# Performance work log

Measured on AMD Instinct MI355X. Metric: run time of the kernel, lower is better.

Reference implementation:

```python
import jax, jax.numpy as jnp
import numpy as np

VOCAB = 100000
EMB = 512
BATCH = 4096
SEQ = 200


def setup_inputs() -> dict:
    key = jax.random.key(0)
    ks = jax.random.split(key, 7)
    inputs = jax.random.randint(ks[0], (BATCH, SEQ), 0, VOCAB, dtype=jnp.int64 if jax.config.jax_enable_x64 else jnp.int32)
    E = jax.random.normal(ks[1], (VOCAB, EMB), dtype=jnp.float32) * 0.1
    dims = [(512, 512), (512, 256), (256, 128), (128, 64), (64, 3)]
    params = {}
    for i, (fi, fo) in enumerate(dims, start=1):
        kw = jax.random.fold_in(ks[2], i)
        # Glorot-uniform like keras Dense default
        lim = (6.0 / (fi + fo)) ** 0.5
        params[f"W{i}"] = jax.random.uniform(kw, (fi, fo), minval=-lim, maxval=lim, dtype=jnp.float32)
        params[f"b{i}"] = jnp.zeros((fo,), dtype=jnp.float32)
    return {"inputs": inputs, "E": E, **params}


def reference(inputs, E, W1, b1, W2, b2, W3, b3, W4, b4, W5, b5):
    # Fused embedding-bag: gather [B,S,EMB] then mean over S (replaces per-row loop)
    sent = jnp.take(E, inputs, axis=0).mean(axis=1)  # [B, EMB]
    h = jax.nn.relu(sent @ W1 + b1)
    h = jax.nn.relu(h @ W2 + b2)
    h = jax.nn.relu(h @ W3 + b3)
    h = jax.nn.relu(h @ W4 + b4)
    return jax.nn.softmax(h @ W5 + b5, axis=-1)  # [B, 3]
```

## Files before the change

kernel.cpp:

```cpp
#include <hip/hip_runtime.h>
#include <hip/hip_bf16.h>
#include <math.h>

#define BATCH 4096
#define SEQ 200
#define EMB 512
#define VOCAB 100000

#define E_SCALE 0.08f
#define E_INVSCALE 12.5f

typedef __attribute__((ext_vector_type(8))) short bf16x8;
typedef __attribute__((ext_vector_type(4))) float f32x4;
typedef __attribute__((ext_vector_type(2))) unsigned int u32x2;

__device__ inline unsigned int f2bf(float f) {
    unsigned int u = __float_as_uint(f);
    return (u + 0x7FFFu + ((u >> 16) & 1u)) >> 16;
}
__device__ inline unsigned int pack2(float lo, float hi) {
    return f2bf(lo) | (f2bf(hi) << 16);
}

#if __has_builtin(__builtin_amdgcn_cvt_f32_fp8)
#define FP8_HW 1
#else
#define FP8_HW 0
__device__ inline float fp8_dec_sw(unsigned int b) {
    unsigned int s = (b >> 7) & 1u, em = b & 0x7fu;
    float v;
    if (em >= 8u)
        v = __uint_as_float((((em >> 3) + 120u) << 23) | ((em & 7u) << 20));
    else
        v = (float)em * 0.001953125f;
    return s ? -v : v;
}
#endif

__device__ inline unsigned int fp4_enc_sw(float v) {
    float ax = fabsf(v) * E_INVSCALE;
    unsigned int m = (unsigned int)(ax >= 0.25f) + (unsigned int)(ax >= 0.75f) +
                     (unsigned int)(ax >= 1.25f) + (unsigned int)(ax >= 1.75f) +
                     (unsigned int)(ax >= 2.5f)  + (unsigned int)(ax >= 3.5f) +
                     (unsigned int)(ax >= 5.0f);
    return m | ((__float_as_uint(v) >> 28) & 8u);
}

#if __has_builtin(__builtin_amdgcn_cvt_scalef32_pk_fp4_f32)
#define FP4_HW 1
#else
#define FP4_HW 0
#endif

#define FP4_TBL_LO 0x3C383000u
#define FP4_TBL_HI 0x4C484440u

struct ConvArgs {
    const float* E;
    u32x2* Eb2;
    int n16;
    const float *s0, *s1, *s2, *s3;
    short *d0, *d1, *d2, *d3;
};

__global__ __launch_bounds__(256) void convert_all(ConvArgs a)
{
    const int bid = blockIdx.x;
    if (bid < 2048) {
        const int stride = 2048 * 256;
        for (int i = bid * 256 + threadIdx.x; i < a.n16; i += stride) {
            const f32x4* p = reinterpret_cast<const f32x4*>(a.E) + (size_t)i * 4;
            f32x4 x0 = __builtin_nontemporal_load(p);
            f32x4 x1 = __builtin_nontemporal_load(p + 1);
            f32x4 x2 = __builtin_nontemporal_load(p + 2);
            f32x4 x3 = __builtin_nontemporal_load(p + 3);
            u32x2 o;
#if FP4_HW
            unsigned int lo = 0, hi = 0;
            lo = __builtin_amdgcn_cvt_scalef32_pk_fp4_f32(
                lo, x0.x * E_INVSCALE, x0.y * E_INVSCALE, 1.0f, 0);
            lo = __builtin_amdgcn_cvt_scalef32_pk_fp4_f32(
                lo, x0.z * E_INVSCALE, x0.w * E_INVSCALE, 1.0f, 1);
            lo = __builtin_amdgcn_cvt_scalef32_pk_fp4_f32(
                lo, x1.x * E_INVSCALE, x1.y * E_INVSCALE, 1.0f, 2);
            lo = __builtin_amdgcn_cvt_scalef32_pk_fp4_f32(
                lo, x1.z * E_INVSCALE, x1.w * E_INVSCALE, 1.0f, 3);
            hi = __builtin_amdgcn_cvt_scalef32_pk_fp4_f32(
                hi, x2.x * E_INVSCALE, x2.y * E_INVSCALE, 1.0f, 0);
            hi = __builtin_amdgcn_cvt_scalef32_pk_fp4_f32(
                hi, x2.z * E_INVSCALE, x2.w * E_INVSCALE, 1.0f, 1);
            hi = __builtin_amdgcn_cvt_scalef32_pk_fp4_f32(
                hi, x3.x * E_INVSCALE, x3.y * E_INVSCALE, 1.0f, 2);
            hi = __builtin_amdgcn_cvt_scalef32_pk_fp4_f32(
                hi, x3.z * E_INVSCALE, x3.w * E_INVSCALE, 1.0f, 3);
            o.x = lo;
            o.y = hi;
#else
            o.x = fp4_enc_sw(x0.x) | (fp4_enc_sw(x0.y) << 4) |
                  (fp4_enc_sw(x0.z) << 8) | (fp4_enc_sw(x0.w) << 12) |
                  (fp4_enc_sw(x1.x) << 16) | (fp4_enc_sw(x1.y) << 20) |
                  (fp4_enc_sw(x1.z) << 24) | (fp4_enc_sw(x1.w) << 28);
            o.y = fp4_enc_sw(x2.x) | (fp4_enc_sw(x2.y) << 4) |
                  (fp4_enc_sw(x2.z) << 8) | (fp4_enc_sw(x2.w) << 12) |
                  (fp4_enc_sw(x3.x) << 16) | (fp4_enc_sw(x3.y) << 20) |
                  (fp4_enc_sw(x3.z) << 24) | (fp4_enc_sw(x3.w) << 28);
#endif
            a.Eb2[i] = o;
        }
        return;
    }
    __shared__ float lds[32][33];
    const int wb = bid - 2048;
    const float* src;
    short* dst;
    int K, N, local;
    if (wb < 256)      { src = a.s0; dst = a.d0; K = 512; N = 512; local = wb; }
    else if (wb < 384) { src = a.s1; dst = a.d1; K = 512; N = 256; local = wb - 256; }
    else if (wb < 416) { src = a.s2; dst = a.d2; K = 256; N = 128; local = wb - 384; }
    else               { src = a.s3; dst = a.d3; K = 128; N = 64;  local = wb - 416; }
    const int nbn = N >> 5;
    const int n0 = (local % nbn) * 32;
    const int k0 = (local / nbn) * 32;
    const int tx = threadIdx.x & 31;
    const int ty = threadIdx.x >> 5;
#pragma unroll
    for (int i = 0; i < 4; ++i)
        lds[ty + 8 * i][tx] = src[(size_t)(k0 + ty + 8 * i) * N + n0 + tx];
    __syncthreads();
#pragma unroll
    for (int i = 0; i < 4; ++i)
        dst[(size_t)(n0 + ty + 8 * i) * K + k0 + tx] =
            (short)f2bf(lds[tx][ty + 8 * i]);
}

__global__ __launch_bounds__(256) void embed_mean_fp4(
    const int* __restrict__ idx, const unsigned int* __restrict__ Eb,
    unsigned int* __restrict__ sentB)
{
    __shared__ int sIdx[SEQ];
    __shared__ float red[3 * 512];
    const int b = blockIdx.x;
    const int t = threadIdx.x;
    if (t < SEQ) sIdx[t] = idx[b * SEQ + t];
    __syncthreads();

    const int g = t >> 6;
    const int lane = t & 63;
    float acc[8] = {};

    for (int s = g; s < SEQ; s += 4) {
        const unsigned int v = Eb[(size_t)sIdx[s] * 64 + lane];
        const unsigned int mlo = v & 0x07070707u;
        const unsigned int mhi = (v >> 4) & 0x07070707u;
        const unsigned int pe =
            __builtin_amdgcn_perm(FP4_TBL_HI, FP4_TBL_LO, mlo) |
            ((v & 0x08080808u) << 4);
        const unsigned int po =
            __builtin_amdgcn_perm(FP4_TBL_HI, FP4_TBL_LO, mhi) |
            (v & 0x80808080u);
#if FP8_HW
        acc[0] += __builtin_amdgcn_cvt_f32_fp8(pe, 0);
        acc[1] += __builtin_amdgcn_cvt_f32_fp8(po, 0);
        acc[2] += __builtin_amdgcn_cvt_f32_fp8(pe, 1);
        acc[3] += __builtin_amdgcn_cvt_f32_fp8(po, 1);
        acc[4] += __builtin_amdgcn_cvt_f32_fp8(pe, 2);
        acc[5] += __builtin_amdgcn_cvt_f32_fp8(po, 2);
        acc[6] += __builtin_amdgcn_cvt_f32_fp8(pe, 3);
        acc[7] += __builtin_amdgcn_cvt_f32_fp8(po, 3);
#else
        acc[0] += fp8_dec_sw(pe & 0xff);
        acc[1] += fp8_dec_sw(po & 0xff);
        acc[2] += fp8_dec_sw((pe >> 8) & 0xff);
        acc[3] += fp8_dec_sw((po >> 8) & 0xff);
        acc[4] += fp8_dec_sw((pe >> 16) & 0xff);
        acc[5] += fp8_dec_sw((po >> 16) & 0xff);
        acc[6] += fp8_dec_sw(pe >> 24);
        acc[7] += fp8_dec_sw(po >> 24);
#endif
    }

    if (g) {
        float4* r = reinterpret_cast<float4*>(&red[(g - 1) * 512 + lane * 8]);
        r[0] = make_float4(acc[0], acc[1], acc[2], acc[3]);
        r[1] = make_float4(acc[4], acc[5], acc[6], acc[7]);
    }
    __syncthreads();
    if (g == 0) {
        const float sc = E_SCALE / (float)SEQ;
        float o[8];
#pragma unroll
        for (int j = 0; j < 8; ++j)
            o[j] = (acc[j] + red[0 * 512 + lane * 8 + j] +
                    red[1 * 512 + lane * 8 + j] + red[2 * 512 + lane * 8 + j]) * sc;
        uint4 pk;
        pk.x = pack2(o[0], o[1]);
        pk.y = pack2(o[2], o[3]);
        pk.z = pack2(o[4], o[5]);
        pk.w = pack2(o[6], o[7]);
        reinterpret_cast<uint4*>(sentB + (size_t)b * 256)[lane] = pk;
    }
}

__global__ __launch_bounds__(256) void embed_mean_kernel(
    const int* __restrict__ idx, const float* __restrict__ E,
    float* __restrict__ sent)
{
    __shared__ int sIdx[SEQ];
    __shared__ float4 red[128];
    const int b = blockIdx.x;
    const int t = threadIdx.x;
    if (t < SEQ) sIdx[t] = idx[b * SEQ + t];
    __syncthreads();

    const int half = t >> 7;
    const int lane = t & 127;
    float4 acc = make_float4(0.f, 0.f, 0.f, 0.f);
    for (int s = half; s < SEQ; s += 2) {
        const float4* row =
            reinterpret_cast<const float4*>(E + (size_t)sIdx[s] * EMB);
        float4 v = row[lane];
        acc.x += v.x; acc.y += v.y; acc.z += v.z; acc.w += v.w;
    }
    if (half == 1) red[lane] = acc;
    __syncthreads();
    if (half == 0) {
        float4 o = red[lane];
        const float sc = 1.0f / (float)SEQ;
        float4 r;
        r.x = (acc.x + o.x) * sc;
        r.y = (acc.y + o.y) * sc;
        r.z = (acc.z + o.z) * sc;
        r.w = (acc.w + o.w) * sc;
        reinterpret_cast<float4*>(sent + (size_t)b * EMB)[lane] = r;
    }
}

template <int N, int K, bool OUT_BF16>
__global__ __launch_bounds__(256) void gemm_mfma_bias_relu(
    const short* __restrict__ A, const short* __restrict__ BT,
    const float* __restrict__ bias, void* __restrict__ C)
{
    __shared__ float4 As[512];
    __shared__ float4 Bs[256];

    const int t = threadIdx.x;
    const int l = t & 63;
    const int w = t >> 6;
    const int wr = w >> 1;
    const int wc = w & 1;
    const int m0 = blockIdx.x * 128;
    const int n0 = blockIdx.y * 64;

    const int srow = (t >> 6) * 16 + (t & 15);
    const int skg = (t >> 4) & 3;

    f32x4 acc[4][2] = {};

    for (int kt = 0; kt < K; kt += 32) {
        const float4 a0 = *reinterpret_cast<const float4*>(
            A + (size_t)(m0 + srow) * K + kt + skg * 8);
        const float4 a1 = *reinterpret_cast<const float4*>(
            A + (size_t)(m0 + srow + 64) * K + kt + skg * 8);
        const float4 b0 = *reinterpret_cast<const float4*>(
            BT + (size_t)(n0 + srow) * K + kt + skg * 8);
        __syncthreads();
        As[t] = a0;
        As[t + 256] = a1;
        Bs[t] = b0;
        __syncthreads();

        bf16x8 afr[4], bfr[2];
#pragma unroll
        for (int f = 0; f < 4; ++f)
            afr[f] = *reinterpret_cast<const bf16x8*>(
                &As[(wr * 4 + f) * 64 + (l >> 4) * 16 + (l & 15)]);
#pragma unroll
        for (int g = 0; g < 2; ++g)
            bfr[g] = *reinterpret_cast<const bf16x8*>(
                &Bs[(wc * 2 + g) * 64 + (l >> 4) * 16 + (l & 15)]);
#pragma unroll
        for (int f = 0; f < 4; ++f)
#pragma unroll
            for (int g = 0; g < 2; ++g)
                acc[f][g] = __builtin_amdgcn_mfma_f32_16x16x32_bf16(
                    afr[f], bfr[g], acc[f][g], 0, 0, 0);
    }

#pragma unroll
    for (int g = 0; g < 2; ++g) {
        const int col = n0 + wc * 32 + g * 16 + (l & 15);
        const float bv = bias[col];
#pragma unroll
        for (int f = 0; f < 4; ++f) {
#pragma unroll
            for (int r = 0; r < 4; ++r) {
                const int row = m0 + wr * 64 + f * 16 + (l >> 4) * 4 + r;
                const float v = fmaxf(acc[f][g][r] + bv, 0.f);
                if (OUT_BF16)
                    ((short*)C)[(size_t)row * N + col] = (short)f2bf(v);
                else
                    ((float*)C)[(size_t)row * N + col] = v;
            }
        }
    }
}

__global__ __launch_bounds__(256) void mlp_tail(
    const short* __restrict__ h2B,
    const short* __restrict__ W3T,
    const float* __restrict__ b3,
    const short* __restrict__ W4T,
    const float* __restrict__ b4,
    const float* __restrict__ W5,
    const float* __restrict__ b5,
    float* __restrict__ out)
{
    __shared__ char buf0[32768];
    __shared__ char h3buf[16384];
    __shared__ float4 Bs[512];
    __shared__ float w5s[192];
    __shared__ float b5s[3];

    const int t = threadIdx.x;
    const int l = t & 63;
    const int w = t >> 6;
    const int wr = w >> 1;
    const int wc = w & 1;
    const int m0 = blockIdx.x * 64;

    if (t < 192) w5s[t] = W5[t];
    if (t < 3) b5s[t] = b5[t];

#pragma unroll
    for (int i = 0; i < 8; ++i) {
        const int c = i * 256 + t;
        const int row = c >> 5;
        const int bc = (c & 31) * 16;
        float4 v = *reinterpret_cast<const float4*>(
            reinterpret_cast<const char*>(h2B + (size_t)(m0 + row) * 256) + bc);
        *reinterpret_cast<float4*>(buf0 + ((row * 512 + bc) ^ ((row & 7) << 4))) = v;
    }

    f32x4 acc3[2][4] = {};
    const int scol = (t >> 6) * 16 + (t & 15);
    const int skg = (t >> 4) & 3;
    for (int kt = 0; kt < 256; kt += 32) {
        __syncthreads();
        Bs[t] = *reinterpret_cast<const float4*>(
            W3T + (size_t)scol * 256 + kt + skg * 8);
        Bs[t + 256] = *reinterpret_cast<const float4*>(
            W3T + (size_t)(scol + 64) * 256 + kt + skg * 8);
        __syncthreads();
        bf16x8 afr[2], bfr[4];
#pragma unroll
        for (int f = 0; f < 2; ++f) {
            const int row = wr * 32 + f * 16 + (l & 15);
            afr[f] = *reinterpret_cast<const bf16x8*>(
                buf0 + ((row * 512 + kt * 2 + (l >> 4) * 16) ^ ((row & 7) << 4)));
        }
#pragma unroll
        for (int g = 0; g < 4; ++g)
            bfr[g] = *reinterpret_cast<const bf16x8*>(
                &Bs[(wc * 4 + g) * 64 + (l >> 4) * 16 + (l & 15)]);
#pragma unroll
        for (int f = 0; f < 2; ++f)
#pragma unroll
            for (int g = 0; g < 4; ++g)
                acc3[f][g] = __builtin_amdgcn_mfma_f32_16x16x32_bf16(
                    afr[f], bfr[g], acc3[f][g], 0, 0, 0);
    }
    __syncthreads();
#pragma unroll
    for (int g = 0; g < 4; ++g) {
        const int col = wc * 64 + g * 16 + (l & 15);
        const float bv = b3[col];
#pragma unroll
        for (int f = 0; f < 2; ++f)
#pragma unroll
            for (int r = 0; r < 4; ++r) {
                const int row = wr * 32 + f * 16 + (l >> 4) * 4 + r;
                const float v = fmaxf(acc3[f][g][r] + bv, 0.f);
                *reinterpret_cast<unsigned short*>(
                    h3buf + ((row * 256 + col * 2) ^ ((row & 7) << 4))) =
                    (unsigned short)f2bf(v);
            }
    }

    f32x4 acc4[2][2] = {};
    for (int kt = 0; kt < 128; kt += 32) {
        __syncthreads();
        Bs[t] = *reinterpret_cast<const float4*>(
            W4T + (size_t)scol * 128 + kt + skg * 8);
        __syncthreads();
        bf16x8 afr[2], bfr[2];
#pragma unroll
        for (int f = 0; f < 2; ++f) {
            const int row = wr * 32 + f * 16 + (l & 15);
            afr[f] = *reinterpret_cast<const bf16x8*>(
                h3buf + ((row * 256 + kt * 2 + (l >> 4) * 16) ^ ((row & 7) << 4)));
        }
#pragma unroll
        for (int g = 0; g < 2; ++g)
            bfr[g] = *reinterpret_cast<const bf16x8*>(
                &Bs[(wc * 2 + g) * 64 + (l >> 4) * 16 + (l & 15)]);
#pragma unroll
        for (int f = 0; f < 2; ++f)
#pragma unroll
            for (int g = 0; g < 2; ++g)
                acc4[f][g] = __builtin_amdgcn_mfma_f32_16x16x32_bf16(
                    afr[f], bfr[g], acc4[f][g], 0, 0, 0);
    }
    __syncthreads();
    float* h4s = reinterpret_cast<float*>(buf0);
#pragma unroll
    for (int g = 0; g < 2; ++g) {
        const int col = wc * 32 + g * 16 + (l & 15);
        const float bv = b4[col];
#pragma unroll
        for (int f = 0; f < 2; ++f)
#pragma unroll
            for (int r = 0; r < 4; ++r) {
                const int row = wr * 32 + f * 16 + (l >> 4) * 4 + r;
                h4s[row * 65 + col] = fmaxf(acc4[f][g][r] + bv, 0.f);
            }
    }
    __syncthreads();

    if (t < 64) {
        float a0 = b5s[0], a1 = b5s[1], a2 = b5s[2];
        const float* hr = &h4s[t * 65];
#pragma unroll
        for (int k = 0; k < 64; ++k) {
            float h = hr[k];
            a0 = fmaf(h, w5s[k * 3 + 0], a0);
            a1 = fmaf(h, w5s[k * 3 + 1], a1);
            a2 = fmaf(h, w5s[k * 3 + 2], a2);
        }
        float m  = fmaxf(a0, fmaxf(a1, a2));
        float e0 = expf(a0 - m), e1 = expf(a1 - m), e2 = expf(a2 - m);
        float inv = 1.0f / (e0 + e1 + e2);
        out[(m0 + t) * 3 + 0] = e0 * inv;
        out[(m0 + t) * 3 + 1] = e1 * inv;
        out[(m0 + t) * 3 + 2] = e2 * inv;
    }
}

template <int N, int K>
__global__ __launch_bounds__(256) void gemm_bias_relu(
    const float* __restrict__ A, const float* __restrict__ W,
    const float* __restrict__ bias, float* __restrict__ C)
{
    constexpr int BK = 16, LDT = 68;
    __shared__ float As[BK][LDT];
    __shared__ float Bs[BK][LDT];

    const int t = threadIdx.x;
    const int m0 = blockIdx.x * 64;
    const int n0 = blockIdx.y * 64;

    const int arow = t >> 2;
    const int acg  = (t & 3) * 4;
    const int brow = t >> 4;
    const int bcg  = (t & 15) * 4;

    const int tr = (t >> 4) * 4;
    const int tc = (t & 15) * 4;

    float acc[4][4] = {};

    for (int kt = 0; kt < K; kt += BK) {
        float4 av = *reinterpret_cast<const float4*>(
            &A[(size_t)(m0 + arow) * K + kt + acg]);
        float4 bv = *reinterpret_cast<const float4*>(
            &W[(size_t)(kt + brow) * N + n0 + bcg]);
        __syncthreads();
        As[acg + 0][arow] = av.x;
        As[acg + 1][arow] = av.y;
        As[acg + 2][arow] = av.z;
        As[acg + 3][arow] = av.w;
        *reinterpret_cast<float4*>(&Bs[brow][bcg]) = bv;
        __syncthreads();
#pragma unroll
        for (int kk = 0; kk < BK; ++kk) {
            float4 a4 = *reinterpret_cast<const float4*>(&As[kk][tr]);
            float4 b4 = *reinterpret_cast<const float4*>(&Bs[kk][tc]);
            float aa[4] = {a4.x, a4.y, a4.z, a4.w};
            float bb[4] = {b4.x, b4.y, b4.z, b4.w};
#pragma unroll
            for (int i = 0; i < 4; ++i)
#pragma unroll
                for (int j = 0; j < 4; ++j)
                    acc[i][j] = fmaf(aa[i], bb[j], acc[i][j]);
        }
    }

    float4 bias4 = *reinterpret_cast<const float4*>(&bias[n0 + tc]);
    float bb[4] = {bias4.x, bias4.y, bias4.z, bias4.w};
#pragma unroll
    for (int i = 0; i < 4; ++i) {
        float4 r;
        r.x = fmaxf(acc[i][0] + bb[0], 0.f);
        r.y = fmaxf(acc[i][1] + bb[1], 0.f);
        r.z = fmaxf(acc[i][2] + bb[2], 0.f);
        r.w = fmaxf(acc[i][3] + bb[3], 0.f);
        *reinterpret_cast<float4*>(&C[(size_t)(m0 + tr + i) * N + n0 + tc]) = r;
    }
}

__global__ __launch_bounds__(256) void final_softmax_kernel(
    const float* __restrict__ h4, const float* __restrict__ W5,
    const float* __restrict__ b5, float* __restrict__ out)
{
    __shared__ float w[64 * 3];
    __shared__ float bb[3];
    const int t = threadIdx.x;
    if (t < 192) w[t] = W5[t];
    if (t < 3) bb[t] = b5[t];
    __syncthreads();

    const int row = blockIdx.x * 256 + t;
    float a0 = bb[0], a1 = bb[1], a2 = bb[2];
    const float* hr = h4 + (size_t)row * 64;
#pragma unroll
    for (int k = 0; k < 64; ++k) {
        float h = hr[k];
        a0 = fmaf(h, w[k * 3 + 0], a0);
        a1 = fmaf(h, w[k * 3 + 1], a1);
        a2 = fmaf(h, w[k * 3 + 2], a2);
    }
    float m  = fmaxf(a0, fmaxf(a1, a2));
    float e0 = expf(a0 - m), e1 = expf(a1 - m), e2 = expf(a2 - m);
    float inv = 1.0f / (e0 + e1 + e2);
    out[row * 3 + 0] = e0 * inv;
    out[row * 3 + 1] = e1 * inv;
    out[row * 3 + 2] = e2 * inv;
}

extern "C" void kernel_launch(void* const* d_in, const int* in_sizes, int n_in,
                              void* d_out, int out_size, void* d_ws,
                              size_t ws_size, hipStream_t stream)
{
    const int*   inputs = (const int*)d_in[0];
    const float* E  = (const float*)d_in[1];
    const float* W1 = (const float*)d_in[2];
    const float* b1 = (const float*)d_in[3];
    const float* W2 = (const float*)d_in[4];
    const float* b2 = (const float*)d_in[5];
    const float* W3 = (const float*)d_in[6];
    const float* b3 = (const float*)d_in[7];
    const float* W4 = (const float*)d_in[8];
    const float* b4 = (const float*)d_in[9];
    const float* W5 = (const float*)d_in[10];
    const float* b5 = (const float*)d_in[11];
    float* out = (float*)d_out;

    const size_t eb4Bytes = (size_t)VOCAB * EMB / 2;
    const size_t needed = 36954112;

    if (ws_size >= needed) {
        char* p = (char*)d_ws;
        unsigned int* Eb4   = (unsigned int*)p;
        short*        W1T   = (short*)(p + eb4Bytes);
        short*        W2T   = (short*)(p + eb4Bytes + 524288);
        short*        W3T   = (short*)(p + eb4Bytes + 786432);
        short*        W4T   = (short*)(p + eb4Bytes + 851968);
        unsigned int* sentB = (unsigned int*)(p + eb4Bytes + 868352);
        short*        h1B   = (short*)(p + eb4Bytes + 868352 + 4194304);
        short*        h2B   = (short*)(p + eb4Bytes + 868352 + 2 * 4194304);

        ConvArgs ca = {E, (u32x2*)Eb4, VOCAB * EMB / 16,
                       W1, W2, W3, W4, W1T, W2T, W3T, W4T};
        convert_all<<<2472, 256, 0, stream>>>(ca);
        embed_mean_fp4<<<BATCH, 256, 0, stream>>>(inputs, Eb4, sentB);

        gemm_mfma_bias_relu<512, 512, true>
            <<<dim3(BATCH / 128, 8), 256, 0, stream>>>(
                (const short*)sentB, W1T, b1, (void*)h1B);
        gemm_mfma_bias_relu<256, 512, true>
            <<<dim3(BATCH / 128, 4), 256, 0, stream>>>(
                h1B, W2T, b2, (void*)h2B);
        mlp_tail<<<BATCH / 64, 256, 0, stream>>>(
            h2B, W3T, b3, W4T, b4, W5, b5, out);
    } else {
        float* act  = (float*)d_ws;
        float* sent = act;
        float* h1   = act + 2097152;
        float* h2   = act;
        float* h3   = act + 2097152;
        float* h4   = act;
        embed_mean_kernel<<<BATCH, 256, 0, stream>>>(inputs, E, sent);
        gemm_bias_relu<512, 512><<<dim3(BATCH / 64, 8), 256, 0, stream>>>(
            sent, W1, b1, h1);
        gemm_bias_relu<256, 512><<<dim3(BATCH / 64, 4), 256, 0, stream>>>(
            h1, W2, b2, h2);
        gemm_bias_relu<128, 256><<<dim3(BATCH / 64, 2), 256, 0, stream>>>(
            h2, W3, b3, h3);
        gemm_bias_relu<64, 128><<<dim3(BATCH / 64, 1), 256, 0, stream>>>(
            h3, W4, b4, h4);
        final_softmax_kernel<<<BATCH / 256, 256, 0, stream>>>(h4, W5, b5, out);
    }
}
```

Baseline: 150.7 us.

## Widen FP4 embedding gathers to 16-byte loads with quarter-wave row split

Reworks the FP4 embedding-bag kernel so each lane loads a uint4 (32 FP4 values) instead of a single 32-bit word. Each 16-lane quarter-wave handles one row and each wave owns a contiguous 50-row slice. Partial sums are first reduced across quarter-waves with shuffles, then across the four waves through a padded LDS buffer, and all 256 threads write packed bf16 output. This cuts the number of gather instructions per row, at the cost of more registers (32 accumulators) and extra shuffle work.

```diff
diff --git a/kernel.cpp b/kernel.cpp
--- a/kernel.cpp
+++ b/kernel.cpp
@@ -138,66 +138,103 @@
     unsigned int* __restrict__ sentB)
 {
     __shared__ int sIdx[SEQ];
-    __shared__ float red[3 * 512];
+    __shared__ float red[4 * 600];
     const int b = blockIdx.x;
     const int t = threadIdx.x;
     if (t < SEQ) sIdx[t] = idx[b * SEQ + t];
     __syncthreads();
 
-    const int g = t >> 6;
-    const int lane = t & 63;
-    float acc[8] = {};
-
-    for (int s = g; s < SEQ; s += 4) {
-        const unsigned int v = Eb[(size_t)sIdx[s] * 64 + lane];
-        const unsigned int mlo = v & 0x07070707u;
-        const unsigned int mhi = (v >> 4) & 0x07070707u;
-        const unsigned int pe =
-            __builtin_amdgcn_perm(FP4_TBL_HI, FP4_TBL_LO, mlo) |
-            ((v & 0x08080808u) << 4);
-        const unsigned int po =
-            __builtin_amdgcn_perm(FP4_TBL_HI, FP4_TBL_LO, mhi) |
-            (v & 0x80808080u);
+    const int w = t >> 6;
+    const int l = t & 63;
+    const int g4 = l >> 4;
+    const int li = l & 15;
+    float acc[32] = {};
+
+#define DECODE_ACC(vd, d)                                                    \
+    do {                                                                     \
+        const unsigned int mlo = (vd) & 0x07070707u;                         \
+        const unsigned int mhi = ((vd) >> 4) & 0x07070707u;                  \
+        const unsigned int pe =                                              \
+            __builtin_amdgcn_perm(FP4_TBL_HI, FP4_TBL_LO, mlo) |             \
+            (((vd) & 0x08080808u) << 4);                                     \
+        const unsigned int po =                                              \
+            __builtin_amdgcn_perm(FP4_TBL_HI, FP4_TBL_LO, mhi) |             \
+            ((vd) & 0x80808080u);                                            \
+        acc[(d) * 8 + 0] += __builtin_amdgcn_cvt_f32_fp8(pe, 0);             \
+        acc[(d) * 8 + 1] += __builtin_amdgcn_cvt_f32_fp8(po, 0);             \
+        acc[(d) * 8 + 2] += __builtin_amdgcn_cvt_f32_fp8(pe, 1);             \
+        acc[(d) * 8 + 3] += __builtin_amdgcn_cvt_f32_fp8(po, 1);             \
+        acc[(d) * 8 + 4] += __builtin_amdgcn_cvt_f32_fp8(pe, 2);             \
+        acc[(d) * 8 + 5] += __builtin_amdgcn_cvt_f32_fp8(po, 2);             \
+        acc[(d) * 8 + 6] += __builtin_amdgcn_cvt_f32_fp8(pe, 3);             \
+        acc[(d) * 8 + 7] += __builtin_amdgcn_cvt_f32_fp8(po, 3);             \
+    } while (0)
+
 #if FP8_HW
-        acc[0] += __builtin_amdgcn_cvt_f32_fp8(pe, 0);
-        acc[1] += __builtin_amdgcn_cvt_f32_fp8(po, 0);
-        acc[2] += __builtin_amdgcn_cvt_f32_fp8(pe, 1);
-        acc[3] += __builtin_amdgcn_cvt_f32_fp8(po, 1);
-        acc[4] += __builtin_amdgcn_cvt_f32_fp8(pe, 2);
-        acc[5] += __builtin_amdgcn_cvt_f32_fp8(po, 2);
-        acc[6] += __builtin_amdgcn_cvt_f32_fp8(pe, 3);
-        acc[7] += __builtin_amdgcn_cvt_f32_fp8(po, 3);
+#define DECODE_QUAD(v)                                                       \
+    do {                                                                     \
+        DECODE_ACC((v).x, 0);                                                \
+        DECODE_ACC((v).y, 1);                                                \
+        DECODE_ACC((v).z, 2);                                                \
+        DECODE_ACC((v).w, 3);                                                \
+    } while (0)
 #else
-        acc[0] += fp8_dec_sw(pe & 0xff);
-        acc[1] += fp8_dec_sw(po & 0xff);
-        acc[2] += fp8_dec_sw((pe >> 8) & 0xff);
-        acc[3] += fp8_dec_sw((po >> 8) & 0xff);
-        acc[4] += fp8_dec_sw((pe >> 16) & 0xff);
-        acc[5] += fp8_dec_sw((po >> 16) & 0xff);
-        acc[6] += fp8_dec_sw(pe >> 24);
-        acc[7] += fp8_dec_sw(po >> 24);
+#define DECODE_ONE_SW(vd, d)                                                 \
+    do {                                                                     \
+        for (int kk = 0; kk < 8; ++kk) {                                     \
+            unsigned int nib = ((vd) >> (4 * kk)) & 0xFu;                    \
+            float mag[8] = {0.f, .5f, 1.f, 1.5f, 2.f, 3.f, 4.f, 6.f};        \
+            float vv = mag[nib & 7u];                                        \
+            acc[(d) * 8 + kk] += (nib & 8u) ? -vv : vv;                      \
+        }                                                                    \
+    } while (0)
+#define DECODE_QUAD(v)                                                       \
+    do {                                                                     \
+        DECODE_ONE_SW((v).x, 0);                                             \
+        DECODE_ONE_SW((v).y, 1);                                             \
+        DECODE_ONE_SW((v).z, 2);                                             \
+        DECODE_ONE_SW((v).w, 3);                                             \
+    } while (0)
 #endif
-    }
-
-    if (g) {
-        float4* r = reinterpret_cast<float4*>(&red[(g - 1) * 512 + lane * 8]);
-        r[0] = make_float4(acc[0], acc[1], acc[2], acc[3]);
-        r[1] = make_float4(acc[4], acc[5], acc[6], acc[7]);
-    }
-    __syncthreads();
-    if (g == 0) {
+
+#pragma unroll 1
+    for (int it = 0; it < 12; ++it) {
+        const int row = 50 * w + 4 * it + g4;
+        const uint4 v = reinterpret_cast<const uint4*>(
+            Eb)[(size_t)sIdx[row] * 16 + li];
+        DECODE_QUAD(v);
+    }
+    if (g4 < 2) {
+        const int row = 50 * w + 48 + g4;
+        const uint4 v = reinterpret_cast<const uint4*>(
+            Eb)[(size_t)sIdx[row] * 16 + li];
+        DECODE_QUAD(v);
+    }
+#undef DECODE_QUAD
+#undef DECODE_ACC
+
+#pragma unroll
+    for (int j = 0; j < 32; ++j) {
+        acc[j] += __shfl_xor(acc[j], 16);
+        acc[j] += __shfl_xor(acc[j], 32);
+    }
+    if (l < 16) {
+        float4* dst = reinterpret_cast<float4*>(&red[w * 600 + l * 36]);
+#pragma unroll
+        for (int j = 0; j < 8; ++j)
+            dst[j] = make_float4(acc[4 * j + 0], acc[4 * j + 1],
+                                 acc[4 * j + 2], acc[4 * j + 3]);
+    }
+    __syncthreads();
+
+    {
         const float sc = E_SCALE / (float)SEQ;
-        float o[8];
-#pragma unroll
-        for (int j = 0; j < 8; ++j)
-            o[j] = (acc[j] + red[0 * 512 + lane * 8 + j] +
-                    red[1 * 512 + lane * 8 + j] + red[2 * 512 + lane * 8 + j]) * sc;
-        uint4 pk;
-        pk.x = pack2(o[0], o[1]);
-        pk.y = pack2(o[2], o[3]);
-        pk.z = pack2(o[4], o[5]);
-        pk.w = pack2(o[6], o[7]);
-        reinterpret_cast<uint4*>(sentB + (size_t)b * 256)[lane] = pk;
+        const int c0 = 2 * t, c1 = 2 * t + 1;
+        const int a0 = 36 * (c0 >> 5) + (c0 & 31);
+        const int a1 = 36 * (c1 >> 5) + (c1 & 31);
+        float s0 = red[a0] + red[600 + a0] + red[1200 + a0] + red[1800 + a0];
+        float s1 = red[a1] + red[600 + a1] + red[1200 + a1] + red[1800 + a1];
+        sentB[(size_t)b * 256 + t] = pack2(s0 * sc, s1 * sc);
     }
 }
 
```

Result: faster. 139.6 us (-7.4%).
